# Kernel tuning notes

Hardware: AMD Instinct MI355X
Metric: run time of the kernel (lower is better)

The kernel has to match this reference:

```python
import jax, jax.numpy as jnp
import numpy as np
from jax import lax

N, E, IN, OUT, H, OH = 2048, 16384, 128, 128, 4, 8
NEG_SLOPE = 0.2

def symlog(v):
    return jnp.sign(v) * jnp.log1p(jnp.abs(v))

def setup_inputs() -> dict:
    key = jax.random.key(0)
    ks = jax.random.split(key, 16)
    x = jax.random.normal(ks[0], (N, IN), dtype=jnp.float32)
    onehot = jax.random.uniform(ks[1], (N, N), dtype=jnp.float32)
    src = jax.random.randint(ks[2], (E,), 0, N, dtype=jnp.int32)
    # guarantee no self loops (original removes them before adding its own)
    off = jax.random.randint(ks[3], (E,), 1, N, dtype=jnp.int32)
    dst = (src + off) % N
    s = 0.05
    lin_w = jax.random.normal(ks[4], (H * OUT, IN + OH), dtype=jnp.float32) * s
    att_l = jax.random.normal(ks[5], (1, H, OUT), dtype=jnp.float32) * s
    att_r = jax.random.normal(ks[6], (1, H, OUT), dtype=jnp.float32) * s
    bias = jnp.zeros((H * OUT,), dtype=jnp.float32)
    conv1_w = jax.random.normal(ks[7], (8, 1, 3), dtype=jnp.float32) * s
    conv1_b = jnp.zeros((8,), dtype=jnp.float32)
    conv2_w = jax.random.normal(ks[8], (16, 8, 3), dtype=jnp.float32) * s
    conv2_b = jnp.zeros((16,), dtype=jnp.float32)
    fc_w = jax.random.normal(ks[9], (OH, 16), dtype=jnp.float32) * s
    fc_b = jnp.zeros((OH,), dtype=jnp.float32)
    return {"x": x, "onehot": onehot, "src": src, "dst": dst,
            "lin_w": lin_w, "att_l": att_l, "att_r": att_r, "bias": bias,
            "conv1_w": conv1_w, "conv1_b": conv1_b, "conv2_w": conv2_w,
            "conv2_b": conv2_b, "fc_w": fc_w, "fc_b": fc_b}

def _forward(x, onehot, src, dst, lin_w, att_l, att_r, bias,
             conv1_w, conv1_b, conv2_w, conv2_b, fc_w, fc_b):
    n = x.shape[0]
    # --- one-hot conv pipeline: sort -> symlog -> Conv1d x2 -> avgpool -> Linear ---
    prep = symlog(jnp.sort(onehot, axis=-1))[:, None, :]          # [N,1,N]
    dn = ('NCH', 'OIH', 'NCH')
    h = lax.conv_general_dilated(prep, conv1_w, (1,), [(1, 1)], dimension_numbers=dn)
    h = jax.nn.relu(h + conv1_b[None, :, None])                    # [N,8,N]
    h = lax.conv_general_dilated(h, conv2_w, (1,), [(1, 1)], dimension_numbers=dn)
    h = jax.nn.relu(h + conv2_b[None, :, None])                    # [N,16,N]
    pooled = h.mean(axis=-1)                                       # AdaptiveAvgPool1d(1) -> [N,16]
    oh_feat = pooled @ fc_w.T + fc_b                               # [N,OH]
    # --- linear + per-head attention logits ---
    xh = (jnp.concatenate([x, oh_feat], axis=-1) @ lin_w.T).reshape(n, H, OUT)
    sa = (xh * att_l).sum(-1)                                      # [N,H]
    ra = (xh * att_r).sum(-1)
    # --- add self loops (input edges contain none) ---
    loop = jnp.arange(n, dtype=src.dtype)
    s_i = jnp.concatenate([src, loop])
    d_i = jnp.concatenate([dst, loop])
    # --- message: LeakyReLU attention * one-hot dot attention ---
    alpha = jax.nn.leaky_relu(sa[s_i] + ra[d_i], NEG_SLOPE)        # [E',H]
    send_oh = onehot[s_i]                                          # [E',N]
    dotatt = 1.0 / ((symlog(send_oh) * symlog(onehot[d_i])).sum(axis=1) + 1.0)
    alpha = alpha * dotatt[:, None]
    # --- segment softmax over receiving node ---
    amax = jax.ops.segment_max(alpha, d_i, num_segments=n)
    ex = jnp.exp(alpha - amax[d_i])
    den = jax.ops.segment_sum(ex, d_i, num_segments=n)
    alpha = ex / (den[d_i] + 1e-16)
    # --- weighted aggregate (scatter-sum) ---
    agg_x = jax.ops.segment_sum(xh[s_i] * alpha[:, :, None], d_i, num_segments=n)
    agg_oh = jax.ops.segment_sum(send_oh, d_i, num_segments=n)
    new_x = agg_x.reshape(n, H * OUT) + bias                       # concat heads + bias
    new_onehot = onehot + agg_oh                                   # one_hot_incay='add'
    return new_x, new_onehot

def reference(x, onehot, src, dst, lin_w, att_l, att_r, bias,
              conv1_w, conv1_b, conv2_w, conv2_b, fc_w, fc_b):
    return _forward(x, onehot, src, dst, lin_w, att_l, att_r, bias,
                    conv1_w, conv1_b, conv2_w, conv2_b, fc_w, fc_b)
```

## Files before the change

kernel.cpp:

```cpp
#include <hip/hip_runtime.h>
#include <math.h>

#define NN   2048
#define NE   16384
#define NET  (NE + NN)
#define INF_ 128
#define OUTF 128
#define NH   4
#define OHF  8
#define NEG_SLOPE 0.2f
#define CAP  512

__device__ __forceinline__ float symlogf_(float v) {
    return copysignf(__logf(1.0f + fabsf(v)), v);
}

__global__ __launch_bounds__(256, 4) void k_sortconv(
    const float* __restrict__ onehot,
    const float* __restrict__ c1w, const float* __restrict__ c1b,
    const float* __restrict__ c2w, const float* __restrict__ c2b,
    const float* __restrict__ fcw, const float* __restrict__ fcb,
    float* __restrict__ slog, float* __restrict__ ohfeat,
    float* __restrict__ datt) {
    __shared__ float soa[NN];
    __shared__ float bndL[4][2];
    __shared__ float bndR[4][2];
    __shared__ float red[64];
    __shared__ float red2[4];
    __shared__ float pooled[16];
    const int t = threadIdx.x;
    const int r = blockIdx.x;
    const int b = t << 3;
    const int wave = t >> 6, lane = t & 63;
    const float* row  = onehot + (size_t)r * NN;
    float*       srow = slog   + (size_t)r * NN;

    float4 lo = ((const float4*)row)[t * 2];
    float4 hi = ((const float4*)row)[t * 2 + 1];
    float v[8] = {lo.x, lo.y, lo.z, lo.w, hi.x, hi.y, hi.z, hi.w};
    {
        float4 s0, s1;
        s0.x = symlogf_(v[0]); s0.y = symlogf_(v[1]);
        s0.z = symlogf_(v[2]); s0.w = symlogf_(v[3]);
        s1.x = symlogf_(v[4]); s1.y = symlogf_(v[5]);
        s1.z = symlogf_(v[6]); s1.w = symlogf_(v[7]);
        ((float4*)srow)[t * 2]     = s0;
        ((float4*)srow)[t * 2 + 1] = s1;
    }

    auto cx = [](float& x, float& y, bool up) {
        float mn = fminf(x, y), mx = fmaxf(x, y);
        x = up ? mn : mx;
        y = up ? mx : mn;
    };

    cx(v[0], v[1], true);  cx(v[2], v[3], false);
    cx(v[4], v[5], true);  cx(v[6], v[7], false);
    cx(v[0], v[2], true);  cx(v[1], v[3], true);
    cx(v[4], v[6], false); cx(v[5], v[7], false);
    cx(v[0], v[1], true);  cx(v[2], v[3], true);
    cx(v[4], v[5], false); cx(v[6], v[7], false);
    {
        const bool u8 = ((t & 1) == 0);
        cx(v[0], v[4], u8); cx(v[1], v[5], u8); cx(v[2], v[6], u8); cx(v[3], v[7], u8);
        cx(v[0], v[2], u8); cx(v[1], v[3], u8); cx(v[4], v[6], u8); cx(v[5], v[7], u8);
        cx(v[0], v[1], u8); cx(v[2], v[3], u8); cx(v[4], v[5], u8); cx(v[6], v[7], u8);
    }

    for (int k = 16; k <= NN; k <<= 1) {
        const bool up = ((b & k) == 0);
        for (int j = k >> 1; j >= 8; j >>= 1) {
            const int pj = j >> 3;
            const bool keepmin = (((t & pj) == 0) == up);
            if (pj <= 32) {
                #pragma unroll
                for (int e = 0; e < 8; e++) {
                    float p = __shfl_xor(v[e], pj, 64);
                    v[e] = keepmin ? fminf(v[e], p) : fmaxf(v[e], p);
                }
            } else {
                __syncthreads();
                #pragma unroll
                for (int e = 0; e < 8; e++) soa[e * 256 + t] = v[e];
                __syncthreads();
                const int pt = t ^ pj;
                #pragma unroll
                for (int e = 0; e < 8; e++) {
                    float p = soa[e * 256 + pt];
                    v[e] = keepmin ? fminf(v[e], p) : fmaxf(v[e], p);
                }
            }
        }
        cx(v[0], v[4], up); cx(v[1], v[5], up); cx(v[2], v[6], up); cx(v[3], v[7], up);
        cx(v[0], v[2], up); cx(v[1], v[3], up); cx(v[4], v[6], up); cx(v[5], v[7], up);
        cx(v[0], v[1], up); cx(v[2], v[3], up); cx(v[4], v[5], up); cx(v[6], v[7], up);
    }

    #pragma unroll
    for (int e = 0; e < 8; e++) v[e] = symlogf_(v[e]);

    float ssq = 0.0f;
    #pragma unroll
    for (int e = 0; e < 8; e++) ssq = fmaf(v[e], v[e], ssq);

    __syncthreads();
    if (lane == 63) { bndL[wave][0] = v[6]; bndL[wave][1] = v[7]; }
    if (lane == 0)  { bndR[wave][0] = v[0]; bndR[wave][1] = v[1]; }
    __syncthreads();
    float vm2 = __shfl_up(v[6], 1, 64);
    float vm1 = __shfl_up(v[7], 1, 64);
    float vp8 = __shfl_down(v[0], 1, 64);
    float vp9 = __shfl_down(v[1], 1, 64);
    if (lane == 0) {
        vm2 = wave ? bndL[wave - 1][0] : 0.0f;
        vm1 = wave ? bndL[wave - 1][1] : 0.0f;
    }
    if (lane == 63) {
        vp8 = (wave < 3) ? bndR[wave + 1][0] : 0.0f;
        vp9 = (wave < 3) ? bndR[wave + 1][1] : 0.0f;
    }

    float vin[12];
    vin[0] = vm2; vin[1] = vm1;
    #pragma unroll
    for (int e = 0; e < 8; e++) vin[2 + e] = v[e];
    vin[10] = vp8; vin[11] = vp9;

    float h1c[10][8];
    {
        float w1[24], b1[8];
        #pragma unroll
        for (int q = 0; q < 24; q++) w1[q] = c1w[q];
        #pragma unroll
        for (int q = 0; q < 8; q++)  b1[q] = c1b[q];
        #pragma unroll
        for (int m = 0; m < 10; m++) {
            const float xm = vin[m], xc = vin[m + 1], xp = vin[m + 2];
            #pragma unroll
            for (int c = 0; c < 8; c++) {
                float a = fmaf(w1[c * 3 + 2], xp,
                          fmaf(w1[c * 3 + 1], xc,
                          fmaf(w1[c * 3 + 0], xm, b1[c])));
                h1c[m][c] = fmaxf(a, 0.0f);
            }
        }
        if (t == 0) {
            #pragma unroll
            for (int c = 0; c < 8; c++) h1c[0][c] = 0.0f;
        }
        if (t == 255) {
            #pragma unroll
            for (int c = 0; c < 8; c++) h1c[9][c] = 0.0f;
        }
    }

    float sums[16];
    #pragma unroll
    for (int ch = 0; ch < 16; ch++) {
        float wch[24];
        #pragma unroll
        for (int q = 0; q < 24; q++) wch[q] = c2w[ch * 24 + q];
        const float bb = c2b[ch];
        float acc = 0.0f;
        #pragma unroll
        for (int i = 0; i < 8; i++) {
            float a = bb;
            #pragma unroll
            for (int c = 0; c < 8; c++) {
                a = fmaf(wch[c * 3 + 0], h1c[i][c],     a);
                a = fmaf(wch[c * 3 + 1], h1c[i + 1][c], a);
                a = fmaf(wch[c * 3 + 2], h1c[i + 2][c], a);
            }
            acc += fmaxf(a, 0.0f);
        }
        sums[ch] = acc;
    }

    #pragma unroll
    for (int c = 0; c < 16; c++)
        for (int o = 32; o; o >>= 1) sums[c] += __shfl_down(sums[c], o);
    #pragma unroll
    for (int o = 32; o; o >>= 1) ssq += __shfl_down(ssq, o);
    if (lane == 0) {
        #pragma unroll
        for (int c = 0; c < 16; c++) red[wave * 16 + c] = sums[c];
        red2[wave] = ssq;
    }
    __syncthreads();
    if (t < 16)
        pooled[t] = (red[t] + red[16 + t] + red[32 + t] + red[48 + t]) * (1.0f / NN);
    if (t == 16)
        datt[NE + r] = 1.0f / (red2[0] + red2[1] + red2[2] + red2[3] + 1.0f);
    __syncthreads();
    if (t < OHF) {
        float a = fcb[t];
        #pragma unroll
        for (int c = 0; c < 16; c++) a = fmaf(fcw[t * 16 + c], pooled[c], a);
        ohfeat[r * OHF + t] = a;
    }
}

__global__ __launch_bounds__(256) void k_xh(
    const float* __restrict__ x, const float* __restrict__ ohf,
    const float* __restrict__ lin_w, const float* __restrict__ att_l,
    const float* __restrict__ att_r, float* __restrict__ xh,
    float* __restrict__ sa, float* __restrict__ ra) {
    const int n0 = blockIdx.x * 4;
    __shared__ float xin[4][136];
    __shared__ float part[4][16];
    const int tid = threadIdx.x;
    const int wave = tid >> 6, lane = tid & 63;
    for (int i = tid; i < 4 * 136; i += 256) {
        int nn = i / 136, k = i - nn * 136;
        xin[nn][k] = (k < INF_) ? x[(size_t)(n0+nn)*INF_ + k]
                                : ohf[(n0+nn)*OHF + (k - INF_)];
    }
    __syncthreads();
    float accl[2][4], accr[2][4];
    #pragma unroll
    for (int g = 0; g < 2; g++)
        #pragma unroll
        for (int n = 0; n < 4; n++) { accl[g][n] = 0.0f; accr[g][n] = 0.0f; }

    #pragma unroll
    for (int g = 0; g < 2; g++) {
        const int o = tid + g * 256;
        const float4* wr4 = (const float4*)(lin_w + (size_t)o * 136);
        float a0 = 0, a1 = 0, a2 = 0, a3 = 0;
        for (int kk = 0; kk < 34; kk++) {
            float4 w = wr4[kk];
            int k = kk * 4;
            a0 += w.x*xin[0][k] + w.y*xin[0][k+1] + w.z*xin[0][k+2] + w.w*xin[0][k+3];
            a1 += w.x*xin[1][k] + w.y*xin[1][k+1] + w.z*xin[1][k+2] + w.w*xin[1][k+3];
            a2 += w.x*xin[2][k] + w.y*xin[2][k+1] + w.z*xin[2][k+2] + w.w*xin[2][k+3];
            a3 += w.x*xin[3][k] + w.y*xin[3][k+1] + w.z*xin[3][k+2] + w.w*xin[3][k+3];
        }
        xh[(size_t)(n0+0)*512 + o] = a0;
        xh[(size_t)(n0+1)*512 + o] = a1;
        xh[(size_t)(n0+2)*512 + o] = a2;
        xh[(size_t)(n0+3)*512 + o] = a3;
        const float al = att_l[o], ar = att_r[o];
        accl[g][0] = fmaf(a0, al, accl[g][0]); accr[g][0] = fmaf(a0, ar, accr[g][0]);
        accl[g][1] = fmaf(a1, al, accl[g][1]); accr[g][1] = fmaf(a1, ar, accr[g][1]);
        accl[g][2] = fmaf(a2, al, accl[g][2]); accr[g][2] = fmaf(a2, ar, accr[g][2]);
        accl[g][3] = fmaf(a3, al, accl[g][3]); accr[g][3] = fmaf(a3, ar, accr[g][3]);
    }
    #pragma unroll
    for (int g = 0; g < 2; g++)
        #pragma unroll
        for (int n = 0; n < 4; n++)
            for (int o = 32; o; o >>= 1) {
                accl[g][n] += __shfl_down(accl[g][n], o);
                accr[g][n] += __shfl_down(accr[g][n], o);
            }
    if (lane == 0) {
        #pragma unroll
        for (int g = 0; g < 2; g++)
            #pragma unroll
            for (int n = 0; n < 4; n++) {
                part[wave][n * 4 + g * 2 + 0] = accl[g][n];
                part[wave][n * 4 + g * 2 + 1] = accr[g][n];
            }
    }
    __syncthreads();
    if (tid < 32) {
        const int n = tid >> 3, rem = tid & 7, h = rem >> 1, lr = rem & 1;
        const int g = h >> 1, wp = (h & 1) * 2;
        const float val = part[wp][n * 4 + g * 2 + lr] + part[wp + 1][n * 4 + g * 2 + lr];
        if (lr == 0) sa[(n0 + n) * 4 + h] = val;
        else         ra[(n0 + n) * 4 + h] = val;
    }
}

__global__ __launch_bounds__(1024) void k_csr(
    const int* __restrict__ dst, int* __restrict__ csr_off,
    int* __restrict__ csr_e) {
    __shared__ int cnt[NN];
    __shared__ int wtot[16];
    const int t = threadIdx.x;
    const int wave = t >> 6, lane = t & 63;
    for (int i = t; i < NN; i += 1024) cnt[i] = 0;
    __syncthreads();
    for (int e = t; e < NET; e += 1024) {
        int d = (e < NE) ? dst[e] : (e - NE);
        atomicAdd(&cnt[d], 1);
    }
    __syncthreads();
    int c0 = cnt[2 * t], c1 = cnt[2 * t + 1];
    int s = c0 + c1;
    int x = s;
    for (int o = 1; o < 64; o <<= 1) {
        int u = __shfl_up(x, o, 64);
        if (lane >= o) x += u;
    }
    if (lane == 63) wtot[wave] = x;
    __syncthreads();
    int off = 0;
    #pragma unroll
    for (int w = 0; w < 16; w++) if (w < wave) off += wtot[w];
    const int base = off + x - s;
    csr_off[2 * t]     = base;
    csr_off[2 * t + 1] = base + c0;
    if (t == 1023) csr_off[NN] = off + x;
    __syncthreads();
    cnt[2 * t]     = base;
    cnt[2 * t + 1] = base + c0;
    __syncthreads();
    for (int e = t; e < NET; e += 1024) {
        int d = (e < NE) ? dst[e] : (e - NE);
        int p = atomicAdd(&cnt[d], 1);
        csr_e[p] = e;
    }
}

__global__ __launch_bounds__(256) void k_datt(
    const int* __restrict__ src, const int* __restrict__ dst,
    const float* __restrict__ slog, float* __restrict__ datt) {
    const int e = blockIdx.x * 4 + (threadIdx.x >> 6);
    const int lane = threadIdx.x & 63;
    const int s = src[e], d = dst[e];
    const float4* A = (const float4*)(slog + (size_t)s * NN);
    const float4* B = (const float4*)(slog + (size_t)d * NN);
    float p = 0.0f;
    #pragma unroll
    for (int i = 0; i < 8; i++) {
        float4 a = A[lane + 64 * i];
        float4 b = B[lane + 64 * i];
        p = fmaf(a.x, b.x, p); p = fmaf(a.y, b.y, p);
        p = fmaf(a.z, b.z, p); p = fmaf(a.w, b.w, p);
    }
    #pragma unroll
    for (int o = 32; o; o >>= 1) p += __shfl_down(p, o);
    if (lane == 0) datt[e] = 1.0f / (p + 1.0f);
}

__global__ __launch_bounds__(256) void k_agg(
    const int* __restrict__ src, const int* __restrict__ csr_off,
    const int* __restrict__ csr_e, const float* __restrict__ datt,
    const float* __restrict__ sa, const float* __restrict__ ra,
    const float* __restrict__ xh, const float* __restrict__ onehot,
    const float* __restrict__ bias, float* __restrict__ out_x,
    float* __restrict__ out_oh) {
    const int d = blockIdx.x;
    const int begin = csr_off[d];
    int deg = csr_off[d + 1] - begin;
    if (deg > CAP) deg = CAP;
    __shared__ float wls[CAP * 4];
    __shared__ int   sls[CAP];
    const int tid = threadIdx.x;
    const float4 rav = *(const float4*)(ra + d * 4);
    for (int t = tid; t < deg; t += 256) {
        int e = csr_e[begin + t];
        int s = (e < NE) ? src[e] : (e - NE);
        sls[t] = s;
        float4 sav = *(const float4*)(sa + s * 4);
        float dt = datt[e];
        float a0 = sav.x + rav.x; a0 = (a0 >= 0.0f ? a0 : NEG_SLOPE * a0) * dt;
        float a1 = sav.y + rav.y; a1 = (a1 >= 0.0f ? a1 : NEG_SLOPE * a1) * dt;
        float a2 = sav.z + rav.z; a2 = (a2 >= 0.0f ? a2 : NEG_SLOPE * a2) * dt;
        float a3 = sav.w + rav.w; a3 = (a3 >= 0.0f ? a3 : NEG_SLOPE * a3) * dt;
        wls[t*4 + 0] = a0; wls[t*4 + 1] = a1;
        wls[t*4 + 2] = a2; wls[t*4 + 3] = a3;
    }
    __syncthreads();
    const int wave = tid >> 6, lane = tid & 63;
    {
        float m = -3.4e38f;
        for (int t = lane; t < deg; t += 64) m = fmaxf(m, wls[t*4 + wave]);
        for (int o = 32; o; o >>= 1) m = fmaxf(m, __shfl_down(m, o));
        m = __shfl(m, 0);
        float s = 0.0f;
        for (int t = lane; t < deg; t += 64) {
            float ex = expf(wls[t*4 + wave] - m);
            wls[t*4 + wave] = ex;
            s += ex;
        }
        for (int o = 32; o; o >>= 1) s += __shfl_down(s, o);
        s = __shfl(s, 0);
        float inv = 1.0f / (s + 1e-16f);
        for (int t = lane; t < deg; t += 64) wls[t*4 + wave] *= inv;
    }
    __syncthreads();
    const int h = tid >> 6;
    float2 accx; accx.x = 0.0f; accx.y = 0.0f;
    const float4* own = (const float4*)(onehot + (size_t)d * NN);
    float4 A = own[tid], B = own[tid + 256];
    const float2* xh2 = (const float2*)xh;
    const float4* oh4 = (const float4*)onehot;
    for (int t = 0; t < deg; t++) {
        const float w = wls[t*4 + h];
        const int s = sls[t];
        float2 xv = xh2[(size_t)s * 256 + tid];
        accx.x = fmaf(w, xv.x, accx.x);
        accx.y = fmaf(w, xv.y, accx.y);
        float4 u  = oh4[(size_t)s * 512 + tid];
        float4 vv = oh4[(size_t)s * 512 + 256 + tid];
        A.x += u.x;  A.y += u.y;  A.z += u.z;  A.w += u.w;
        B.x += vv.x; B.y += vv.y; B.z += vv.z; B.w += vv.w;
    }
    float2 bv = ((const float2*)bias)[tid];
    float2 outv; outv.x = accx.x + bv.x; outv.y = accx.y + bv.y;
    ((float2*)out_x)[(size_t)d * 256 + tid] = outv;
    float4* o4 = (float4*)(out_oh + (size_t)d * NN);
    o4[tid] = A; o4[tid + 256] = B;
}

extern "C" void kernel_launch(void* const* d_in, const int* in_sizes, int n_in,
                              void* d_out, int out_size, void* d_ws, size_t ws_size,
                              hipStream_t stream) {
    const float* x      = (const float*)d_in[0];
    const float* onehot = (const float*)d_in[1];
    const int*   src    = (const int*)d_in[2];
    const int*   dst    = (const int*)d_in[3];
    const float* lin_w  = (const float*)d_in[4];
    const float* att_l  = (const float*)d_in[5];
    const float* att_r  = (const float*)d_in[6];
    const float* bias   = (const float*)d_in[7];
    const float* c1w    = (const float*)d_in[8];
    const float* c1b    = (const float*)d_in[9];
    const float* c2w    = (const float*)d_in[10];
    const float* c2b    = (const float*)d_in[11];
    const float* fcw    = (const float*)d_in[12];
    const float* fcb    = (const float*)d_in[13];

    float* out_x  = (float*)d_out;
    float* out_oh = out_x + (size_t)NN * (NH * OUTF);

    float* ws    = (float*)d_ws;
    float* slog  = ws;
    float* xh    = slog + (size_t)NN * NN;
    float* ohf   = xh   + (size_t)NN * 512;
    float* sa    = ohf  + (size_t)NN * OHF;
    float* ra    = sa   + (size_t)NN * NH;
    float* datt  = ra   + (size_t)NN * NH;
    int* csr_off = (int*)(datt + (size_t)NET);
    int* csr_e   = csr_off + NN + 1;

    k_sortconv<<<NN, 256, 0, stream>>>(onehot, c1w, c1b, c2w, c2b, fcw, fcb,
                                       slog, ohf, datt);
    k_csr<<<1, 1024, 0, stream>>>(dst, csr_off, csr_e);
    k_xh<<<NN / 4, 256, 0, stream>>>(x, ohf, lin_w, att_l, att_r, xh, sa, ra);
    k_datt<<<NE / 4, 256, 0, stream>>>(src, dst, slog, datt);
    k_agg<<<NN, 256, 0, stream>>>(src, csr_off, csr_e, datt, sa, ra, xh, onehot,
                                  bias, out_x, out_oh);
}
```

Before: 286.2 us.

## Fuse dot-attention into aggregation kernel and drop symlog matrix materialization

The per-edge symlog dot-product attention moves from a separate kernel into the aggregation kernel. Neighbor onehot rows are already loaded there for the onehot sum, so symlog is recomputed on the fly instead of being read from a materialized N×N symlog buffer. This removes the 16 MB symlog write in the sort/conv kernel, the extra full-row reads in the datt kernel, and one launch. In exchange it adds per-neighbor transcendental work and a wave reduction with an LDS write inside the aggregation loop. Self loops are handled by doubling the own row and using the own squared norm.

```diff
diff --git a/kernel.cpp b/kernel.cpp
--- a/kernel.cpp
+++ b/kernel.cpp
@@ -20,33 +20,21 @@
     const float* __restrict__ c1w, const float* __restrict__ c1b,
     const float* __restrict__ c2w, const float* __restrict__ c2b,
     const float* __restrict__ fcw, const float* __restrict__ fcb,
-    float* __restrict__ slog, float* __restrict__ ohfeat,
-    float* __restrict__ datt) {
+    float* __restrict__ ohfeat) {
     __shared__ float soa[NN];
     __shared__ float bndL[4][2];
     __shared__ float bndR[4][2];
     __shared__ float red[64];
-    __shared__ float red2[4];
     __shared__ float pooled[16];
     const int t = threadIdx.x;
     const int r = blockIdx.x;
     const int b = t << 3;
     const int wave = t >> 6, lane = t & 63;
-    const float* row  = onehot + (size_t)r * NN;
-    float*       srow = slog   + (size_t)r * NN;
+    const float* row = onehot + (size_t)r * NN;
 
     float4 lo = ((const float4*)row)[t * 2];
     float4 hi = ((const float4*)row)[t * 2 + 1];
     float v[8] = {lo.x, lo.y, lo.z, lo.w, hi.x, hi.y, hi.z, hi.w};
-    {
-        float4 s0, s1;
-        s0.x = symlogf_(v[0]); s0.y = symlogf_(v[1]);
-        s0.z = symlogf_(v[2]); s0.w = symlogf_(v[3]);
-        s1.x = symlogf_(v[4]); s1.y = symlogf_(v[5]);
-        s1.z = symlogf_(v[6]); s1.w = symlogf_(v[7]);
-        ((float4*)srow)[t * 2]     = s0;
-        ((float4*)srow)[t * 2 + 1] = s1;
-    }
 
     auto cx = [](float& x, float& y, bool up) {
         float mn = fminf(x, y), mx = fmaxf(x, y);
@@ -99,10 +87,6 @@
     #pragma unroll
     for (int e = 0; e < 8; e++) v[e] = symlogf_(v[e]);
 
-    float ssq = 0.0f;
-    #pragma unroll
-    for (int e = 0; e < 8; e++) ssq = fmaf(v[e], v[e], ssq);
-
     __syncthreads();
     if (lane == 63) { bndL[wave][0] = v[6]; bndL[wave][1] = v[7]; }
     if (lane == 0)  { bndR[wave][0] = v[0]; bndR[wave][1] = v[1]; }
@@ -179,18 +163,12 @@
     #pragma unroll
     for (int c = 0; c < 16; c++)
         for (int o = 32; o; o >>= 1) sums[c] += __shfl_down(sums[c], o);
-    #pragma unroll
-    for (int o = 32; o; o >>= 1) ssq += __shfl_down(ssq, o);
-    if (lane == 0) {
+    if (lane == 0)
         #pragma unroll
         for (int c = 0; c < 16; c++) red[wave * 16 + c] = sums[c];
-        red2[wave] = ssq;
-    }
     __syncthreads();
     if (t < 16)
         pooled[t] = (red[t] + red[16 + t] + red[32 + t] + red[48 + t]) * (1.0f / NN);
-    if (t == 16)
-        datt[NE + r] = 1.0f / (red2[0] + red2[1] + red2[2] + red2[3] + 1.0f);
     __syncthreads();
     if (t < OHF) {
         float a = fcb[t];
@@ -313,48 +291,68 @@
     }
 }
 
-__global__ __launch_bounds__(256) void k_datt(
-    const int* __restrict__ src, const int* __restrict__ dst,
-    const float* __restrict__ slog, float* __restrict__ datt) {
-    const int e = blockIdx.x * 4 + (threadIdx.x >> 6);
-    const int lane = threadIdx.x & 63;
-    const int s = src[e], d = dst[e];
-    const float4* A = (const float4*)(slog + (size_t)s * NN);
-    const float4* B = (const float4*)(slog + (size_t)d * NN);
-    float p = 0.0f;
-    #pragma unroll
-    for (int i = 0; i < 8; i++) {
-        float4 a = A[lane + 64 * i];
-        float4 b = B[lane + 64 * i];
-        p = fmaf(a.x, b.x, p); p = fmaf(a.y, b.y, p);
-        p = fmaf(a.z, b.z, p); p = fmaf(a.w, b.w, p);
-    }
-    #pragma unroll
-    for (int o = 32; o; o >>= 1) p += __shfl_down(p, o);
-    if (lane == 0) datt[e] = 1.0f / (p + 1.0f);
-}
-
 __global__ __launch_bounds__(256) void k_agg(
     const int* __restrict__ src, const int* __restrict__ csr_off,
-    const int* __restrict__ csr_e, const float* __restrict__ datt,
-    const float* __restrict__ sa, const float* __restrict__ ra,
-    const float* __restrict__ xh, const float* __restrict__ onehot,
-    const float* __restrict__ bias, float* __restrict__ out_x,
-    float* __restrict__ out_oh) {
+    const int* __restrict__ csr_e, const float* __restrict__ sa,
+    const float* __restrict__ ra, const float* __restrict__ xh,
+    const float* __restrict__ onehot, const float* __restrict__ bias,
+    float* __restrict__ out_x, float* __restrict__ out_oh) {
     const int d = blockIdx.x;
     const int begin = csr_off[d];
     int deg = csr_off[d + 1] - begin;
     if (deg > CAP) deg = CAP;
+    __shared__ float pw[4][CAP];
     __shared__ float wls[CAP * 4];
     __shared__ int   sls[CAP];
     const int tid = threadIdx.x;
+    const int wave = tid >> 6, lane = tid & 63;
+
+    for (int t = tid; t < deg; t += 256) {
+        int e = csr_e[begin + t];
+        sls[t] = (e < NE) ? src[e] : d;
+    }
+
+    const float4* oh4 = (const float4*)onehot;
+    float4 ownA = oh4[(size_t)d * 512 + tid];
+    float4 ownB = oh4[(size_t)d * 512 + 256 + tid];
+    float4 sA, sB;
+    sA.x = symlogf_(ownA.x); sA.y = symlogf_(ownA.y);
+    sA.z = symlogf_(ownA.z); sA.w = symlogf_(ownA.w);
+    sB.x = symlogf_(ownB.x); sB.y = symlogf_(ownB.y);
+    sB.z = symlogf_(ownB.z); sB.w = symlogf_(ownB.w);
+    float4 A, B;
+    A.x = 2.0f*ownA.x; A.y = 2.0f*ownA.y; A.z = 2.0f*ownA.z; A.w = 2.0f*ownA.w;
+    B.x = 2.0f*ownB.x; B.y = 2.0f*ownB.y; B.z = 2.0f*ownB.z; B.w = 2.0f*ownB.w;
+    __syncthreads();
+
+    for (int t = 0; t < deg; t++) {
+        const int s = sls[t];
+        float p;
+        if (s == d) {
+            p = sA.x*sA.x + sA.y*sA.y + sA.z*sA.z + sA.w*sA.w
+              + sB.x*sB.x + sB.y*sB.y + sB.z*sB.z + sB.w*sB.w;
+        } else {
+            float4 u  = oh4[(size_t)s * 512 + tid];
+            float4 vv = oh4[(size_t)s * 512 + 256 + tid];
+            A.x += u.x;  A.y += u.y;  A.z += u.z;  A.w += u.w;
+            B.x += vv.x; B.y += vv.y; B.z += vv.z; B.w += vv.w;
+            p = symlogf_(u.x)*sA.x + symlogf_(u.y)*sA.y
+              + symlogf_(u.z)*sA.z + symlogf_(u.w)*sA.w
+              + symlogf_(vv.x)*sB.x + symlogf_(vv.y)*sB.y
+              + symlogf_(vv.z)*sB.z + symlogf_(vv.w)*sB.w;
+        }
+        #pragma unroll
+        for (int o = 32; o; o >>= 1) p += __shfl_down(p, o);
+        if (lane == 0) pw[wave][t] = p;
+    }
+    __syncthreads();
+
     const float4 rav = *(const float4*)(ra + d * 4);
     for (int t = tid; t < deg; t += 256) {
-        int e = csr_e[begin + t];
-        int s = (e < NE) ? src[e] : (e - NE);
-        sls[t] = s;
+        const float dot = pw[0][t] + pw[1][t] + pw[2][t] + pw[3][t];
+        const float dt  = 1.0f / (dot + 1.0f);
+        const int s = sls[t];
         float4 sav = *(const float4*)(sa + s * 4);
-        float dt = datt[e];
         float a0 = sav.x + rav.x; a0 = (a0 >= 0.0f ? a0 : NEG_SLOPE * a0) * dt;
         float a1 = sav.y + rav.y; a1 = (a1 >= 0.0f ? a1 : NEG_SLOPE * a1) * dt;
         float a2 = sav.z + rav.z; a2 = (a2 >= 0.0f ? a2 : NEG_SLOPE * a2) * dt;
@@ -363,7 +361,7 @@
         wls[t*4 + 2] = a2; wls[t*4 + 3] = a3;
     }
     __syncthreads();
-    const int wave = tid >> 6, lane = tid & 63;
+
     {
         float m = -3.4e38f;
         for (int t = lane; t < deg; t += 64) m = fmaxf(m, wls[t*4 + wave]);
@@ -381,22 +379,16 @@
         for (int t = lane; t < deg; t += 64) wls[t*4 + wave] *= inv;
     }
     __syncthreads();
+
     const int h = tid >> 6;
     float2 accx; accx.x = 0.0f; accx.y = 0.0f;
-    const float4* own = (const float4*)(onehot + (size_t)d * NN);
-    float4 A = own[tid], B = own[tid + 256];
     const float2* xh2 = (const float2*)xh;
-    const float4* oh4 = (const float4*)onehot;
     for (int t = 0; t < deg; t++) {
         const float w = wls[t*4 + h];
         const int s = sls[t];
         float2 xv = xh2[(size_t)s * 256 + tid];
         accx.x = fmaf(w, xv.x, accx.x);
         accx.y = fmaf(w, xv.y, accx.y);
-        float4 u  = oh4[(size_t)s * 512 + tid];
-        float4 vv = oh4[(size_t)s * 512 + 256 + tid];
-        A.x += u.x;  A.y += u.y;  A.z += u.z;  A.w += u.w;
-        B.x += vv.x; B.y += vv.y; B.z += vv.z; B.w += vv.w;
     }
     float2 bv = ((const float2*)bias)[tid];
     float2 outv; outv.x = accx.x + bv.x; outv.y = accx.y + bv.y;
@@ -427,20 +419,16 @@
     float* out_oh = out_x + (size_t)NN * (NH * OUTF);
 
     float* ws    = (float*)d_ws;
-    float* slog  = ws;
-    float* xh    = slog + (size_t)NN * NN;
-    float* ohf   = xh   + (size_t)NN * 512;
-    float* sa    = ohf  + (size_t)NN * OHF;
-    float* ra    = sa   + (size_t)NN * NH;
-    float* datt  = ra   + (size_t)NN * NH;
-    int* csr_off = (int*)(datt + (size_t)NET);
+    float* xh    = ws;
+    float* ohf   = xh  + (size_t)NN * 512;
+    float* sa    = ohf + (size_t)NN * OHF;
+    float* ra    = sa  + (size_t)NN * NH;
+    int* csr_off = (int*)(ra + (size_t)NN * NH);
     int* csr_e   = csr_off + NN + 1;
 
-    k_sortconv<<<NN, 256, 0, stream>>>(onehot, c1w, c1b, c2w, c2b, fcw, fcb,
-                                       slog, ohf, datt);
+    k_sortconv<<<NN, 256, 0, stream>>>(onehot, c1w, c1b, c2w, c2b, fcw, fcb, ohf);
     k_csr<<<1, 1024, 0, stream>>>(dst, csr_off, csr_e);
     k_xh<<<NN / 4, 256, 0, stream>>>(x, ohf, lin_w, att_l, att_r, xh, sa, ra);
-    k_datt<<<NE / 4, 256, 0, stream>>>(src, dst, slog, datt);
-    k_agg<<<NN, 256, 0, stream>>>(src, csr_off, csr_e, datt, sa, ra, xh, onehot,
+    k_agg<<<NN, 256, 0, stream>>>(src, csr_off, csr_e, sa, ra, xh, onehot,
                                   bias, out_x, out_oh);
 }
```

Measured after the change: 260.1 us. 9.1% less time.
